# Kernel optimization log

Measured on AMD Instinct MI355X. Metric: run time of the kernel, lower is better.

Reference implementation:

```python
import jax, jax.numpy as jnp
import numpy as np

DIM = 768
NUM_HEADS = 12
HEAD_DIM = DIM // NUM_HEADS
SCALE = HEAD_DIM ** -0.5


def setup_inputs() -> dict:
    key = jax.random.key(0)
    ks = jax.random.split(key, 6)
    B, N, C = 4, 2048, DIM
    x = jax.random.normal(ks[0], (B, N, C), dtype=jnp.float32)
    qkv_weight = jax.random.normal(ks[1], (3 * C, C), dtype=jnp.float32) * (C ** -0.5)
    q_bias = jax.random.normal(ks[2], (C,), dtype=jnp.float32) * 0.02
    v_bias = jax.random.normal(ks[3], (C,), dtype=jnp.float32) * 0.02
    proj_weight = jax.random.normal(ks[4], (C, C), dtype=jnp.float32) * (C ** -0.5)
    proj_bias = jax.random.normal(ks[5], (C,), dtype=jnp.float32) * 0.02
    return {"x": x, "qkv_weight": qkv_weight, "q_bias": q_bias,
            "v_bias": v_bias, "proj_weight": proj_weight, "proj_bias": proj_bias}


def reference(x, qkv_weight, q_bias, v_bias, proj_weight, proj_bias):
    B, N, C = x.shape
    # bias = concat(q_bias, zeros_like(v_bias), v_bias)
    bias = jnp.concatenate([q_bias, jnp.zeros_like(v_bias), v_bias])
    qkv = x @ qkv_weight.T + bias                      # [B, N, 3C]
    qkv = qkv.reshape(B, N, 3, NUM_HEADS, HEAD_DIM)
    q, k, v = jnp.moveaxis(qkv, 2, 0)                  # each [B, N, H, hd]
    q = jnp.transpose(q, (0, 2, 1, 3)) * SCALE         # [B, H, N, hd]
    k = jnp.transpose(k, (0, 2, 1, 3))
    v = jnp.transpose(v, (0, 2, 1, 3))
    attn = jax.nn.softmax(jnp.einsum('bhqd,bhkd->bhqk', q, k), axis=-1)
    out = jnp.einsum('bhqk,bhkd->bhqd', attn, v)       # [B, H, N, hd]
    out = jnp.transpose(out, (0, 2, 1, 3)).reshape(B, N, C)
    return out @ proj_weight.T + proj_bias
```

## Files before the change

kernel.cpp:

```cpp
#include <hip/hip_runtime.h>
#include <cstdint>
#include <cstddef>

typedef _Float16 f16;
typedef _Float16 f16x8 __attribute__((ext_vector_type(8)));
typedef _Float16 f16x4 __attribute__((ext_vector_type(4)));
typedef __fp16 h16x2 __attribute__((ext_vector_type(2)));
typedef float f32x4 __attribute__((ext_vector_type(4)));

#define DIM 768
#define NHEAD 12
#define HD 64
#define BATCH 4
#define SEQ 2048
#define MROWS (BATCH*SEQ)
#define C3 (3*DIM)
#define NBH (BATCH*NHEAD)

__device__ __forceinline__ f32x4 mfma32(f16x8 a, f16x8 b, f32x4 c) {
  return __builtin_amdgcn_mfma_f32_16x16x32_f16(a, b, c, 0, 0, 0);
}
__device__ __forceinline__ f32x4 mfma16(f16x4 a, f16x4 b, f32x4 c) {
  return __builtin_amdgcn_mfma_f32_16x16x16f16(a, b, c, 0, 0, 0);
}

__device__ __forceinline__ void gl2lds16(const void* g, void* l) {
  __builtin_amdgcn_global_load_lds(
      (const __attribute__((address_space(1))) void*)g,
      (__attribute__((address_space(3))) void*)l, 16, 0, 0);
}

__global__ __launch_bounds__(256) void k_convert(
    const float* __restrict__ x, const float* __restrict__ wqkv,
    const float* __restrict__ wproj,
    f16* __restrict__ xh, f16* __restrict__ wqh, f16* __restrict__ wph)
{
  const int NX = MROWS*DIM/4, NW = C3*DIM/4;
  int i = blockIdx.x * 256 + threadIdx.x;
  const float4* src; f16* dst; int idx;
  if (i < NX)         { src = (const float4*)x;     dst = xh;  idx = i; }
  else if (i < NX+NW) { src = (const float4*)wqkv;  dst = wqh; idx = i - NX; }
  else                { src = (const float4*)wproj; dst = wph; idx = i - NX - NW; }
  float4 v = src[idx];
  union { f16 h[4]; uint64_t u; } r;
  r.h[0] = (f16)v.x; r.h[1] = (f16)v.y; r.h[2] = (f16)v.z; r.h[3] = (f16)v.w;
  ((uint64_t*)dst)[idx] = r.u;
}

__device__ __forceinline__ void gemm_tile(
    const f16* __restrict__ A, const f16* __restrict__ B,
    int lda, int ldb, int K, int am0, int bn0,
    f16* smem, f32x4 acc[4][4])
{
  f16* sA0 = smem;         f16* sA1 = smem + 4096;
  f16* sB0 = smem + 8192;  f16* sB1 = smem + 12288;
  const int tid = threadIdx.x, wid = tid >> 6;
  const int lane = tid & 63, lane15 = lane & 15, quad = lane >> 4;
  const int wm = wid >> 1, wn = wid & 1;

  auto stage = [&](int k0, f16* sA, f16* sB) {
    #pragma unroll
    for (int i = 0; i < 2; i++) {
      int j = i*256 + tid;
      int row = j >> 2;
      int sc  = (j & 3) ^ ((row >> 1) & 3);
      gl2lds16(A + (size_t)(am0 + row)*lda + k0 + sc*8, sA + (i*256 + wid*64)*8);
      gl2lds16(B + (size_t)(bn0 + row)*ldb + k0 + sc*8, sB + (i*256 + wid*64)*8);
    }
  };

  const int NK = K >> 5;
  stage(0, sA0, sB0);
  for (int kk = 0; kk < NK; kk++) {
    f16* cA = (kk & 1) ? sA1 : sA0;
    f16* cB = (kk & 1) ? sB1 : sB0;
    __syncthreads();
    if (kk + 1 < NK)
      stage((kk + 1) << 5, (kk & 1) ? sA0 : sA1, (kk & 1) ? sB0 : sB1);
    f16x8 af[4], bf[4];
    #pragma unroll
    for (int t = 0; t < 4; t++) {
      int ra = wm*64 + t*16 + lane15;
      af[t] = *(const f16x8*)(cA + ra*32 + ((quad ^ ((ra >> 1) & 3)) << 3));
      int rb = wn*64 + t*16 + lane15;
      bf[t] = *(const f16x8*)(cB + rb*32 + ((quad ^ ((rb >> 1) & 3)) << 3));
    }
    #pragma unroll
    for (int mt = 0; mt < 4; mt++)
      #pragma unroll
      for (int nt = 0; nt < 4; nt++)
        acc[mt][nt] = mfma32(af[mt], bf[nt], acc[mt][nt]);
  }
}

__device__ __forceinline__ void gemm_tile_128x64(
    const f16* __restrict__ A, const f16* __restrict__ B,
    int lda, int ldb, int K, int am0, int bn0,
    f16* smem, f32x4 acc[4][2])
{
  f16* sA0 = smem;         f16* sA1 = smem + 4096;
  f16* sB0 = smem + 8192;  f16* sB1 = smem + 10240;
  const int tid = threadIdx.x, wid = tid >> 6;
  const int lane = tid & 63, lane15 = lane & 15, quad = lane >> 4;
  const int wm = wid >> 1, wn = wid & 1;

  auto stage = [&](int k0, f16* sA, f16* sB) {
    #pragma unroll
    for (int i = 0; i < 2; i++) {
      int j = i*256 + tid;
      int row = j >> 2;
      int sc  = (j & 3) ^ ((row >> 1) & 3);
      gl2lds16(A + (size_t)(am0 + row)*lda + k0 + sc*8, sA + (i*256 + wid*64)*8);
    }
    int rowb = tid >> 2;
    int scb  = (tid & 3) ^ ((rowb >> 1) & 3);
    gl2lds16(B + (size_t)(bn0 + rowb)*ldb + k0 + scb*8, sB + (wid*64)*8);
  };

  const int NK = K >> 5;
  stage(0, sA0, sB0);
  for (int kk = 0; kk < NK; kk++) {
    f16* cA = (kk & 1) ? sA1 : sA0;
    f16* cB = (kk & 1) ? sB1 : sB0;
    __syncthreads();
    if (kk + 1 < NK)
      stage((kk + 1) << 5, (kk & 1) ? sA0 : sA1, (kk & 1) ? sB0 : sB1);
    f16x8 af[4], bf[2];
    #pragma unroll
    for (int t = 0; t < 4; t++) {
      int ra = wm*64 + t*16 + lane15;
      af[t] = *(const f16x8*)(cA + ra*32 + ((quad ^ ((ra >> 1) & 3)) << 3));
    }
    #pragma unroll
    for (int t = 0; t < 2; t++) {
      int rb = wn*32 + t*16 + lane15;
      bf[t] = *(const f16x8*)(cB + rb*32 + ((quad ^ ((rb >> 1) & 3)) << 3));
    }
    #pragma unroll
    for (int mt = 0; mt < 4; mt++)
      #pragma unroll
      for (int nt = 0; nt < 2; nt++)
        acc[mt][nt] = mfma32(af[mt], bf[nt], acc[mt][nt]);
  }
}

__global__ __launch_bounds__(256, 4) void k_qkv(
    const f16* __restrict__ xh, const f16* __restrict__ wqh,
    const float* __restrict__ q_bias, const float* __restrict__ v_bias,
    f16* __restrict__ Qh, f16* __restrict__ Kh, f16* __restrict__ Vt)
{
  __shared__ f16 smem[16384];
  f32x4 acc[4][4];
  const f32x4 z4 = {0.f, 0.f, 0.f, 0.f};
  #pragma unroll
  for (int a = 0; a < 4; a++)
    #pragma unroll
    for (int b = 0; b < 4; b++) acc[a][b] = z4;

  const int tid = threadIdx.x, wid = tid >> 6, lane = tid & 63;
  const int lane15 = lane & 15, quad = lane >> 4;
  const int wm = wid >> 1, wn = wid & 1;
  const int cblk = blockIdx.x * 128;
  const int mblk = blockIdx.y * 128;
  const int bb = mblk >> 11, nbase = mblk & (SEQ - 1);
  const float QS = 0.125f * 1.4426950408889634f;

  if (cblk < 2*DIM) {
    gemm_tile(wqh, xh, DIM, DIM, DIM, cblk, mblk, smem, acc);
    const bool isQ = (cblk < DIM);
    #pragma unroll
    for (int mt = 0; mt < 4; mt++) {
      int c0 = cblk + wm*64 + mt*16 + quad*4;
      int cr = isQ ? c0 : (c0 - DIM);
      int h = cr >> 6, d0 = cr & 63;
      float4 qb4 = isQ ? *(const float4*)(q_bias + c0) : make_float4(0,0,0,0);
      f16* dst = isQ ? Qh : Kh;
      f16* base = dst + (((size_t)(bb*NHEAD + h)*SEQ + nbase) << 6) + d0;
      #pragma unroll
      for (int nt = 0; nt < 4; nt++) {
        int n = wn*64 + nt*16 + lane15;
        f32x4 v = acc[mt][nt];
        f16x4 hv;
        if (isQ) {
          hv[0] = (f16)((v[0] + qb4.x) * QS); hv[1] = (f16)((v[1] + qb4.y) * QS);
          hv[2] = (f16)((v[2] + qb4.z) * QS); hv[3] = (f16)((v[3] + qb4.w) * QS);
        } else {
          hv[0] = (f16)v[0]; hv[1] = (f16)v[1]; hv[2] = (f16)v[2]; hv[3] = (f16)v[3];
        }
        *(f16x4*)(base + ((size_t)n << 6)) = hv;
      }
    }
  } else {
    gemm_tile(xh, wqh, DIM, DIM, DIM, mblk, cblk, smem, acc);
    #pragma unroll
    for (int nt = 0; nt < 4; nt++) {
      int c = cblk + wn*64 + nt*16 + lane15;
      int c2 = c - 2*DIM;
      int h = c2 >> 6, d = c2 & 63;
      float b = v_bias[c2];
      f16* base = Vt + ((size_t)(bb*NHEAD + h)*HD + d)*SEQ + nbase;
      #pragma unroll
      for (int mt = 0; mt < 4; mt++) {
        int n0 = wm*64 + mt*16 + quad*4;
        f32x4 v = acc[mt][nt];
        f16x4 hv = {(f16)(v[0]+b), (f16)(v[1]+b), (f16)(v[2]+b), (f16)(v[3]+b)};
        *(f16x4*)(base + n0) = hv;
      }
    }
  }
}

#define KVT 128
#define NIT (SEQ/KVT)
__global__ __launch_bounds__(128, 2) void k_attn(
    const f16* __restrict__ Qh, const f16* __restrict__ Kh,
    const f16* __restrict__ Vt, f16* __restrict__ attnh)
{
  __shared__ f16 smem[2*8192 + 64*132];
  f16* sK0 = smem;
  f16* sK1 = smem + 8192;
  f16* sV  = smem + 16384;

  const int tid = threadIdx.x, wid = tid >> 6, lane = tid & 63;
  const int lane15 = lane & 15, quad = lane >> 4;
  const int q0 = blockIdx.x * 128;
  const int bh = blockIdx.y;
  const int qw = q0 + wid*64;

  const f16* Kbh = Kh + (size_t)bh*SEQ*HD;
  const f16* Vbh = Vt + (size_t)bh*HD*SEQ;

  f16x8 qf[4][2];
  #pragma unroll
  for (int qt = 0; qt < 4; qt++)
    #pragma unroll
    for (int ks = 0; ks < 2; ks++)
      qf[qt][ks] = *(const f16x8*)(Qh + ((size_t)bh*SEQ + qw + qt*16 + lane15)*HD
                                      + ks*32 + quad*8);

  f32x4 o[4][4];
  f32x4 sacc[4];
  const f32x4 z4 = {0.f, 0.f, 0.f, 0.f};
  #pragma unroll
  for (int dt = 0; dt < 4; dt++)
    #pragma unroll
    for (int qt = 0; qt < 4; qt++) o[dt][qt] = z4;
  #pragma unroll
  for (int qt = 0; qt < 4; qt++) sacc[qt] = z4;
  const f16x4 one4 = {(f16)1.f, (f16)1.f, (f16)1.f, (f16)1.f};

  const int vrow = tid >> 1, vcg = (tid & 1) * 64;
  const f16* vsrc = Vbh + (size_t)vrow*SEQ + vcg;

  auto stageK = [&](int kv0, f16* sK) {
    #pragma unroll
    for (int i = 0; i < 8; i++) {
      int j = i*128 + tid;
      int row = j >> 3;
      int sc  = (j & 7) ^ (row & 7);
      gl2lds16(Kbh + (size_t)(kv0 + row)*HD + sc*8, sK + (i*128 + wid*64)*8);
    }
  };

  stageK(0, sK0);
  f16x8 vreg[8];
  #pragma unroll
  for (int j = 0; j < 8; j++) vreg[j] = *(const f16x8*)(vsrc + j*8);

  for (int it = 0; it < NIT; it++) {
    f16* cK = (it & 1) ? sK1 : sK0;
    __syncthreads();
    #pragma unroll
    for (int j = 0; j < 8; j++) {
      union { f16x8 v; f16x4 h[2]; } u; u.v = vreg[j];
      *(f16x4*)(sV + vrow*132 + vcg + j*8)     = u.h[0];
      *(f16x4*)(sV + vrow*132 + vcg + j*8 + 4) = u.h[1];
    }
    __syncthreads();
    if (it + 1 < NIT) {
      stageK((it + 1)*KVT, (it & 1) ? sK0 : sK1);
      #pragma unroll
      for (int j = 0; j < 8; j++)
        vreg[j] = *(const f16x8*)(vsrc + (it + 1)*KVT + j*8);
    }

    #pragma unroll
    for (int c = 0; c < 4; c++) {
      f16x8 ka[2][2];
      #pragma unroll
      for (int kt = 0; kt < 2; kt++) {
        int rb = c*32 + kt*16 + lane15;
        #pragma unroll
        for (int ks = 0; ks < 2; ks++)
          ka[ks][kt] = *(const f16x8*)(cK + rb*64 + (((ks*4 + quad) ^ (rb & 7)) << 3));
      }
      f32x4 s[2][4];
      #pragma unroll
      for (int kt = 0; kt < 2; kt++)
        #pragma unroll
        for (int qt = 0; qt < 4; qt++) s[kt][qt] = z4;
      #pragma unroll
      for (int ks = 0; ks < 2; ks++)
        #pragma unroll
        for (int kt = 0; kt < 2; kt++)
          #pragma unroll
          for (int qt = 0; qt < 4; qt++)
            s[kt][qt] = mfma32(ka[ks][kt], qf[qt][ks], s[kt][qt]);

      f16x4 pb[2][4];
      #pragma unroll
      for (int kt = 0; kt < 2; kt++)
        #pragma unroll
        for (int qt = 0; qt < 4; qt++) {
          union { h16x2 g2[2]; f16x4 h4; } u;
          u.g2[0] = __builtin_amdgcn_cvt_pkrtz(exp2f(s[kt][qt][0]), exp2f(s[kt][qt][1]));
          u.g2[1] = __builtin_amdgcn_cvt_pkrtz(exp2f(s[kt][qt][2]), exp2f(s[kt][qt][3]));
          pb[kt][qt] = u.h4;
        }
      #pragma unroll
      for (int kt = 0; kt < 2; kt++)
        #pragma unroll
        for (int qt = 0; qt < 4; qt++)
          sacc[qt] = mfma16(one4, pb[kt][qt], sacc[qt]);

      #pragma unroll
      for (int dt = 0; dt < 4; dt++) {
        int row = dt*16 + lane15;
        #pragma unroll
        for (int kt = 0; kt < 2; kt++) {
          int c16 = 4*c + 2*kt + (quad >> 1);
          f16x4 va = *(const f16x4*)(sV + row*132 + c16*8 + (quad & 1)*4);
          #pragma unroll
          for (int qt = 0; qt < 4; qt++)
            o[dt][qt] = mfma16(va, pb[kt][qt], o[dt][qt]);
        }
      }
    }
  }

  float inv[4];
  #pragma unroll
  for (int qt = 0; qt < 4; qt++) inv[qt] = 1.f / sacc[qt][0];

  __syncthreads();
  f16* tb = smem + wid * (64 * 72);
  #pragma unroll
  for (int dt = 0; dt < 4; dt++)
    #pragma unroll
    for (int qt = 0; qt < 4; qt++) {
      f32x4 v = o[dt][qt];
      float iv = inv[qt];
      f16x4 hx = {(f16)(v[0]*iv), (f16)(v[1]*iv), (f16)(v[2]*iv), (f16)(v[3]*iv)};
      *(f16x4*)(tb + (qt*16 + lane15)*72 + dt*16 + quad*4) = hx;
    }
  const int b = bh / NHEAD, h = bh % NHEAD;
  #pragma unroll
  for (int i = 0; i < 8; i++) {
    int row = i*8 + (lane >> 3);
    f16x8 rv = *(const f16x8*)(tb + row*72 + (lane & 7)*8);
    *(f16x8*)(attnh + ((size_t)b*SEQ + qw + row)*DIM + h*HD + (lane & 7)*8) = rv;
  }
}

__global__ __launch_bounds__(256, 3) void k_proj(
    const f16* __restrict__ ah, const f16* __restrict__ wph,
    const float* __restrict__ pbias, float* __restrict__ out)
{
  __shared__ f16 smem[12288];
  f32x4 acc[4][2];
  const f32x4 z4 = {0.f, 0.f, 0.f, 0.f};
  #pragma unroll
  for (int a = 0; a < 4; a++)
    #pragma unroll
    for (int b = 0; b < 2; b++) acc[a][b] = z4;

  const int cblk = blockIdx.y * 128;
  const int mblk = blockIdx.x * 64;
  gemm_tile_128x64(wph, ah, DIM, DIM, DIM, cblk, mblk, smem, acc);

  const int tid = threadIdx.x, wid = tid >> 6, lane = tid & 63;
  const int lane15 = lane & 15, quad = lane >> 4;
  const int wm = wid >> 1, wn = wid & 1;
  #pragma unroll
  for (int mt = 0; mt < 4; mt++) {
    int c0 = cblk + wm*64 + mt*16 + quad*4;
    float4 b4 = *(const float4*)(pbias + c0);
    #pragma unroll
    for (int nt = 0; nt < 2; nt++) {
      int m = mblk + wn*32 + nt*16 + lane15;
      f32x4 v = acc[mt][nt];
      float4 r = make_float4(v[0]+b4.x, v[1]+b4.y, v[2]+b4.z, v[3]+b4.w);
      *(float4*)(out + (size_t)m*DIM + c0) = r;
    }
  }
}

extern "C" void kernel_launch(void* const* d_in, const int* in_sizes, int n_in,
                              void* d_out, int out_size, void* d_ws, size_t ws_size,
                              hipStream_t stream) {
  const float* x    = (const float*)d_in[0];
  const float* wqkv = (const float*)d_in[1];
  const float* qb   = (const float*)d_in[2];
  const float* vb   = (const float*)d_in[3];
  const float* wp   = (const float*)d_in[4];
  const float* pb   = (const float*)d_in[5];
  float* out = (float*)d_out;

  f16* p = (f16*)d_ws;
  f16* xh  = p; p += (size_t)MROWS*DIM;
  f16* wqh = p; p += (size_t)C3*DIM;
  f16* wph = p; p += (size_t)DIM*DIM;
  f16* Qh  = p; p += (size_t)NBH*SEQ*HD;
  f16* Kh  = p; p += (size_t)NBH*SEQ*HD;
  f16* Vt  = p; p += (size_t)NBH*SEQ*HD;
  f16* attnh = xh;

  k_convert<<<8448, 256, 0, stream>>>(x, wqkv, wp, xh, wqh, wph);
  k_qkv<<<dim3(C3/128, MROWS/128), 256, 0, stream>>>(xh, wqh, qb, vb, Qh, Kh, Vt);
  k_attn<<<dim3(SEQ/128, NBH), 128, 0, stream>>>(Qh, Kh, Vt, attnh);
  k_proj<<<dim3(MROWS/64, DIM/128), 256, 0, stream>>>(attnh, wph, pb, out);
}
```

Measured before the change: 265.2 us.

## Remap blocks to XCDs for L2 locality and widen attention blocks to four waves

All three kernels now use a 1D grid and remap block IDs so that blocks sharing the same input rows, or the same batch-head for attention, land on the same XCD, improving L2 reuse across MI355X's chiplets. The attention kernel also goes from 2 waves of 64 queries to 4 waves of 32 queries per block. Each block still covers 128 queries, but per-wave register use is halved, so more waves can be resident (launch bounds 256,3). The trade-off is that K/V LDS traffic is amortized over fewer queries per wave. An extra barrier is added before the output readback.

```diff
diff --git a/kernel.cpp b/kernel.cpp
--- a/kernel.cpp
+++ b/kernel.cpp
@@ -160,8 +160,9 @@
   const int tid = threadIdx.x, wid = tid >> 6, lane = tid & 63;
   const int lane15 = lane & 15, quad = lane >> 4;
   const int wm = wid >> 1, wn = wid & 1;
-  const int cblk = blockIdx.x * 128;
-  const int mblk = blockIdx.y * 128;
+  const int id = blockIdx.x, xcd = id & 7, j = id >> 3;
+  const int cblk = (j % 18) * 128;
+  const int mblk = (xcd + 8 * (j / 18)) * 128;
   const int bb = mblk >> 11, nbase = mblk & (SEQ - 1);
   const float QS = 0.125f * 1.4426950408889634f;
 
@@ -212,7 +213,7 @@
 
 #define KVT 128
 #define NIT (SEQ/KVT)
-__global__ __launch_bounds__(128, 2) void k_attn(
+__global__ __launch_bounds__(256, 3) void k_attn(
     const f16* __restrict__ Qh, const f16* __restrict__ Kh,
     const f16* __restrict__ Vt, f16* __restrict__ attnh)
 {
@@ -223,65 +224,65 @@
 
   const int tid = threadIdx.x, wid = tid >> 6, lane = tid & 63;
   const int lane15 = lane & 15, quad = lane >> 4;
-  const int q0 = blockIdx.x * 128;
-  const int bh = blockIdx.y;
-  const int qw = q0 + wid*64;
+  const int id = blockIdx.x, xcd = id & 7, j = id >> 3;
+  const int bh = xcd * 6 + (j >> 4);
+  const int q0 = (j & 15) * 128;
+  const int qw = q0 + wid*32;
 
   const f16* Kbh = Kh + (size_t)bh*SEQ*HD;
   const f16* Vbh = Vt + (size_t)bh*HD*SEQ;
 
-  f16x8 qf[4][2];
-  #pragma unroll
-  for (int qt = 0; qt < 4; qt++)
+  f16x8 qf[2][2];
+  #pragma unroll
+  for (int qt = 0; qt < 2; qt++)
     #pragma unroll
     for (int ks = 0; ks < 2; ks++)
       qf[qt][ks] = *(const f16x8*)(Qh + ((size_t)bh*SEQ + qw + qt*16 + lane15)*HD
                                       + ks*32 + quad*8);
 
-  f32x4 o[4][4];
-  f32x4 sacc[4];
+  f32x4 o[4][2];
+  f32x4 sacc[2];
   const f32x4 z4 = {0.f, 0.f, 0.f, 0.f};
   #pragma unroll
   for (int dt = 0; dt < 4; dt++)
     #pragma unroll
-    for (int qt = 0; qt < 4; qt++) o[dt][qt] = z4;
-  #pragma unroll
-  for (int qt = 0; qt < 4; qt++) sacc[qt] = z4;
+    for (int qt = 0; qt < 2; qt++) o[dt][qt] = z4;
+  sacc[0] = z4; sacc[1] = z4;
   const f16x4 one4 = {(f16)1.f, (f16)1.f, (f16)1.f, (f16)1.f};
 
-  const int vrow = tid >> 1, vcg = (tid & 1) * 64;
+  const int vrow = tid >> 2, vcg = (tid & 3) * 32;
   const f16* vsrc = Vbh + (size_t)vrow*SEQ + vcg;
 
   auto stageK = [&](int kv0, f16* sK) {
     #pragma unroll
-    for (int i = 0; i < 8; i++) {
-      int j = i*128 + tid;
-      int row = j >> 3;
-      int sc  = (j & 7) ^ (row & 7);
-      gl2lds16(Kbh + (size_t)(kv0 + row)*HD + sc*8, sK + (i*128 + wid*64)*8);
+    for (int i = 0; i < 4; i++) {
+      int j2 = i*256 + tid;
+      int row = j2 >> 3;
+      int sc  = (j2 & 7) ^ (row & 7);
+      gl2lds16(Kbh + (size_t)(kv0 + row)*HD + sc*8, sK + (i*256 + wid*64)*8);
     }
   };
 
   stageK(0, sK0);
-  f16x8 vreg[8];
-  #pragma unroll
-  for (int j = 0; j < 8; j++) vreg[j] = *(const f16x8*)(vsrc + j*8);
+  f16x8 vreg[4];
+  #pragma unroll
+  for (int j2 = 0; j2 < 4; j2++) vreg[j2] = *(const f16x8*)(vsrc + j2*8);
 
   for (int it = 0; it < NIT; it++) {
     f16* cK = (it & 1) ? sK1 : sK0;
     __syncthreads();
     #pragma unroll
-    for (int j = 0; j < 8; j++) {
-      union { f16x8 v; f16x4 h[2]; } u; u.v = vreg[j];
-      *(f16x4*)(sV + vrow*132 + vcg + j*8)     = u.h[0];
-      *(f16x4*)(sV + vrow*132 + vcg + j*8 + 4) = u.h[1];
+    for (int j2 = 0; j2 < 4; j2++) {
+      union { f16x8 v; f16x4 h[2]; } u; u.v = vreg[j2];
+      *(f16x4*)(sV + vrow*132 + vcg + j2*8)     = u.h[0];
+      *(f16x4*)(sV + vrow*132 + vcg + j2*8 + 4) = u.h[1];
     }
     __syncthreads();
     if (it + 1 < NIT) {
       stageK((it + 1)*KVT, (it & 1) ? sK0 : sK1);
       #pragma unroll
-      for (int j = 0; j < 8; j++)
-        vreg[j] = *(const f16x8*)(vsrc + (it + 1)*KVT + j*8);
+      for (int j2 = 0; j2 < 4; j2++)
+        vreg[j2] = *(const f16x8*)(vsrc + (it + 1)*KVT + j2*8);
     }
 
     #pragma unroll
@@ -294,24 +295,24 @@
         for (int ks = 0; ks < 2; ks++)
           ka[ks][kt] = *(const f16x8*)(cK + rb*64 + (((ks*4 + quad) ^ (rb & 7)) << 3));
       }
-      f32x4 s[2][4];
+      f32x4 s[2][2];
       #pragma unroll
       for (int kt = 0; kt < 2; kt++)
         #pragma unroll
-        for (int qt = 0; qt < 4; qt++) s[kt][qt] = z4;
+        for (int qt = 0; qt < 2; qt++) s[kt][qt] = z4;
       #pragma unroll
       for (int ks = 0; ks < 2; ks++)
         #pragma unroll
         for (int kt = 0; kt < 2; kt++)
           #pragma unroll
-          for (int qt = 0; qt < 4; qt++)
+          for (int qt = 0; qt < 2; qt++)
             s[kt][qt] = mfma32(ka[ks][kt], qf[qt][ks], s[kt][qt]);
 
-      f16x4 pb[2][4];
+      f16x4 pb[2][2];
       #pragma unroll
       for (int kt = 0; kt < 2; kt++)
         #pragma unroll
-        for (int qt = 0; qt < 4; qt++) {
+        for (int qt = 0; qt < 2; qt++) {
           union { h16x2 g2[2]; f16x4 h4; } u;
           u.g2[0] = __builtin_amdgcn_cvt_pkrtz(exp2f(s[kt][qt][0]), exp2f(s[kt][qt][1]));
           u.g2[1] = __builtin_amdgcn_cvt_pkrtz(exp2f(s[kt][qt][2]), exp2f(s[kt][qt][3]));
@@ -320,7 +321,7 @@
       #pragma unroll
       for (int kt = 0; kt < 2; kt++)
         #pragma unroll
-        for (int qt = 0; qt < 4; qt++)
+        for (int qt = 0; qt < 2; qt++)
           sacc[qt] = mfma16(one4, pb[kt][qt], sacc[qt]);
 
       #pragma unroll
@@ -331,31 +332,30 @@
           int c16 = 4*c + 2*kt + (quad >> 1);
           f16x4 va = *(const f16x4*)(sV + row*132 + c16*8 + (quad & 1)*4);
           #pragma unroll
-          for (int qt = 0; qt < 4; qt++)
+          for (int qt = 0; qt < 2; qt++)
             o[dt][qt] = mfma16(va, pb[kt][qt], o[dt][qt]);
         }
       }
     }
   }
 
-  float inv[4];
-  #pragma unroll
-  for (int qt = 0; qt < 4; qt++) inv[qt] = 1.f / sacc[qt][0];
+  float inv[2] = {1.f / sacc[0][0], 1.f / sacc[1][0]};
 
   __syncthreads();
-  f16* tb = smem + wid * (64 * 72);
+  f16* tb = smem + wid * (32 * 72);
   #pragma unroll
   for (int dt = 0; dt < 4; dt++)
     #pragma unroll
-    for (int qt = 0; qt < 4; qt++) {
+    for (int qt = 0; qt < 2; qt++) {
       f32x4 v = o[dt][qt];
       float iv = inv[qt];
       f16x4 hx = {(f16)(v[0]*iv), (f16)(v[1]*iv), (f16)(v[2]*iv), (f16)(v[3]*iv)};
       *(f16x4*)(tb + (qt*16 + lane15)*72 + dt*16 + quad*4) = hx;
     }
+  __syncthreads();
   const int b = bh / NHEAD, h = bh % NHEAD;
   #pragma unroll
-  for (int i = 0; i < 8; i++) {
+  for (int i = 0; i < 4; i++) {
     int row = i*8 + (lane >> 3);
     f16x8 rv = *(const f16x8*)(tb + row*72 + (lane & 7)*8);
     *(f16x8*)(attnh + ((size_t)b*SEQ + qw + row)*DIM + h*HD + (lane & 7)*8) = rv;
@@ -374,8 +374,9 @@
     #pragma unroll
     for (int b = 0; b < 2; b++) acc[a][b] = z4;
 
-  const int cblk = blockIdx.y * 128;
-  const int mblk = blockIdx.x * 64;
+  const int id = blockIdx.x, xcd = id & 7, j = id >> 3;
+  const int cblk = (j % 6) * 128;
+  const int mblk = (xcd + 8 * (j / 6)) * 64;
   gemm_tile_128x64(wph, ah, DIM, DIM, DIM, cblk, mblk, smem, acc);
 
   const int tid = threadIdx.x, wid = tid >> 6, lane = tid & 63;
@@ -416,7 +417,7 @@
   f16* attnh = xh;
 
   k_convert<<<8448, 256, 0, stream>>>(x, wqkv, wp, xh, wqh, wph);
-  k_qkv<<<dim3(C3/128, MROWS/128), 256, 0, stream>>>(xh, wqh, qb, vb, Qh, Kh, Vt);
-  k_attn<<<dim3(SEQ/128, NBH), 128, 0, stream>>>(Qh, Kh, Vt, attnh);
-  k_proj<<<dim3(MROWS/64, DIM/128), 256, 0, stream>>>(attnh, wph, pb, out);
-}
+  k_qkv<<<1152, 256, 0, stream>>>(xh, wqh, qb, vb, Qh, Kh, Vt);
+  k_attn<<<768, 256, 0, stream>>>(Qh, Kh, Vt, attnh);
+  k_proj<<<768, 256, 0, stream>>>(attnh, wph, pb, out);
+}
```

After: 236.5 us. 10.8% less time.
